# Kernel tuning notes

Hardware: AMD Instinct MI355X
Metric: run time of the kernel (lower is better)

Reference implementation:

```python
import jax, jax.numpy as jnp
import numpy as np

N, L, D = 4, 2048, 1024
H_DIM, OUT_DIM = 1024, 1024


def setup_inputs() -> dict:
    key = jax.random.key(0)
    ks = jax.random.split(key, 7)
    scale = 0.02
    return {
        "x": jax.random.normal(ks[0], (N, L, D), dtype=jnp.float32),
        "Wq": jax.random.normal(ks[1], (D, H_DIM), dtype=jnp.float32) * scale,
        "bq": jnp.zeros((H_DIM,), dtype=jnp.float32),
        "Wk": jax.random.normal(ks[2], (D, H_DIM), dtype=jnp.float32) * scale,
        "bk": jnp.zeros((H_DIM,), dtype=jnp.float32),
        "Wv": jax.random.normal(ks[3], (D, OUT_DIM), dtype=jnp.float32) * scale,
        "bv": jnp.zeros((OUT_DIM,), dtype=jnp.float32),
    }


def reference(x, Wq, bq, Wk, bk, Wv, bv):
    # q,k: [N,L,h_dim], v: [N,L,out_dim]
    q = jnp.einsum("nld,dh->nlh", x, Wq) + bq
    k = jnp.einsum("nld,dh->nlh", x, Wk) + bk
    v = jnp.einsum("nld,do->nlo", x, Wv) + bv
    # scores: [N,L,L]
    qk = jnp.einsum("nlh,nmh->nlm", q, k)
    # NOTE: original scales by sqrt(qk.shape[-1]) == sqrt(L) (seq len), not sqrt(h_dim)
    seq_len = qk.shape[-1]
    s = jax.nn.softmax(qk / jnp.sqrt(jnp.asarray(seq_len, dtype=qk.dtype)), axis=-1)
    return jnp.einsum("nlm,nmo->nlo", s, v)
```

## Files before the change

kernel.cpp:

```cpp
#include <hip/hip_runtime.h>
#include <hip/hip_bf16.h>


typedef __attribute__((ext_vector_type(8))) short bf16x8;
typedef __attribute__((ext_vector_type(4))) float f32x4;

#define AS_G(p) ((__attribute__((address_space(1))) void*)(p))
#define AS_L(p) ((__attribute__((address_space(3))) void*)(p))

__device__ __forceinline__ unsigned short f2bf(float f) {
  unsigned int u = __float_as_uint(f);
  unsigned int lsb = (u >> 16) & 1u;
  u += 0x7fffu + lsb;
  return (unsigned short)(u >> 16);
}

__device__ __forceinline__ float bf2f(unsigned short h) {
  return __uint_as_float(((unsigned int)h) << 16);
}


template <int EPI>
__global__ __launch_bounds__(256) void gemm64(
    const unsigned short* __restrict__ A, const unsigned short* __restrict__ B,
    float* __restrict__ Cf, long long sA, long long sB, long long sC,
    int K, int lda, int ldb, int ldc,
    unsigned short* __restrict__ u0, unsigned short* __restrict__ u1,
    unsigned short* __restrict__ u2,
    const float* __restrict__ f0, const float* __restrict__ f1,
    const float* __restrict__ f2,
    float* __restrict__ rsum, float scale)
{
  __shared__ unsigned short lA[128 * 64];
  __shared__ unsigned short lB[128 * 64];

  const int t = threadIdx.x;
  const int rowBase = blockIdx.y * 128;
  const int colBase = blockIdx.x * 128;
  A += (long long)blockIdx.z * sA;
  B += (long long)blockIdx.z * sB;

  const int l = t & 63;
  const int w = t >> 6;
  const int wrow = (w >> 1) * 64;
  const int wcol = (w & 1) * 64;
  const int q = l >> 4;
  const int r16 = l & 15;

  f32x4 acc[4][4] = {};

  const int r0 = t >> 3;
  const int goff = (((t & 7) ^ (r0 & 7)) << 3);

  for (int kt = 0; kt < K; kt += 64) {
    __syncthreads();
#pragma unroll
    for (int u = 0; u < 4; u++) {
      const int row = r0 + 32 * u;
      __builtin_amdgcn_global_load_lds(AS_G(A + (size_t)(rowBase + row) * lda + kt + goff),
                                       AS_L(lA + (t + 256 * u) * 8), 16, 0, 0);
      __builtin_amdgcn_global_load_lds(AS_G(B + (size_t)(colBase + row) * ldb + kt + goff),
                                       AS_L(lB + (t + 256 * u) * 8), 16, 0, 0);
    }
    __syncthreads();

#pragma unroll
    for (int ks = 0; ks < 2; ks++) {
      bf16x8 af[4], bfr[4];
#pragma unroll
      for (int i = 0; i < 4; i++) {
        const int s = ((ks * 4 + q) ^ (r16 & 7));
        af[i] = *(const bf16x8*)(lA + (wrow + i * 16 + r16) * 64 + s * 8);
      }
#pragma unroll
      for (int j = 0; j < 4; j++) {
        const int s = ((ks * 4 + q) ^ (r16 & 7));
        bfr[j] = *(const bf16x8*)(lB + (wcol + j * 16 + r16) * 64 + s * 8);
      }
#pragma unroll
      for (int i = 0; i < 4; i++)
#pragma unroll
        for (int j = 0; j < 4; j++)
          acc[i][j] = __builtin_amdgcn_mfma_f32_16x16x32_bf16(af[i], bfr[j], acc[i][j], 0, 0, 0);
    }
  }

  if (EPI == 1) {
    unsigned short* p16 = u0 + (long long)blockIdx.z * sC;
    float* rs = rsum + (long long)blockIdx.z * 2048;
#pragma unroll
    for (int i = 0; i < 4; i++) {
#pragma unroll
      for (int r = 0; r < 4; r++) {
        int row = rowBase + wrow + i * 16 + q * 4 + r;
        float rowpart = 0.f;
#pragma unroll
        for (int j = 0; j < 4; j++) {
          int col = colBase + wcol + j * 16 + r16;
          float e = __expf(acc[i][j][r] * scale);
          p16[(size_t)row * ldc + col] = f2bf(e);
          rowpart += e;
        }
#pragma unroll
        for (int m = 1; m < 16; m <<= 1) rowpart += __shfl_xor(rowpart, m);
        if (r16 == 0) atomicAdd(rs + row, rowpart);
      }
    }
  } else if (EPI == 2) {
    const int seg = colBase >> 10;
    if (seg < 2) {
      unsigned short* dst = seg ? u1 : u0;
      const float* bias = seg ? f1 : f0;
      const int cb = colBase & 1023;
#pragma unroll
      for (int i = 0; i < 4; i++) {
#pragma unroll
        for (int r = 0; r < 4; r++) {
          int row = rowBase + wrow + i * 16 + q * 4 + r;
#pragma unroll
          for (int j = 0; j < 4; j++) {
            int col = cb + wcol + j * 16 + r16;
            dst[(size_t)row * 1024 + col] = f2bf(acc[i][j][r] + bias[col]);
          }
        }
      }
    } else {
      const int ob = colBase - 2048;
#pragma unroll
      for (int i = 0; i < 4; i++) {
        int posBase = rowBase + wrow + i * 16 + q * 4;
        int b = posBase >> 11;
        int pos = posBase & 2047;
#pragma unroll
        for (int j = 0; j < 4; j++) {
          int o = ob + wcol + j * 16 + r16;
          float bias = f2[o];
          ushort4 pk;
          pk.x = f2bf(acc[i][j][0] + bias);
          pk.y = f2bf(acc[i][j][1] + bias);
          pk.z = f2bf(acc[i][j][2] + bias);
          pk.w = f2bf(acc[i][j][3] + bias);
          *(ushort4*)(u2 + ((size_t)((b << 10) + o) * 2048 + pos)) = pk;
        }
      }
    }
  } else {
    float* C = Cf + (long long)blockIdx.z * sC;
    const float* rs = rsum + (long long)blockIdx.z * 2048;
#pragma unroll
    for (int i = 0; i < 4; i++) {
#pragma unroll
      for (int r = 0; r < 4; r++) {
        int row = rowBase + wrow + i * 16 + q * 4 + r;
        float inv = 1.0f / rs[row];
#pragma unroll
        for (int j = 0; j < 4; j++) {
          int col = colBase + wcol + j * 16 + r16;
          C[(size_t)row * ldc + col] = acc[i][j][r] * inv;
        }
      }
    }
  }
}


__global__ __launch_bounds__(256) void cast_f32_to_bf16(
    const float* __restrict__ in, unsigned short* __restrict__ out, int n4,
    float* __restrict__ rzero, int nz4)
{
  int i = blockIdx.x * 256 + threadIdx.x;
  if (i < nz4) ((float4*)rzero)[i] = make_float4(0.f, 0.f, 0.f, 0.f);
  if (i >= n4) return;
  float4 v = ((const float4*)in)[i];
  ushort4 o;
  o.x = f2bf(v.x); o.y = f2bf(v.y); o.z = f2bf(v.z); o.w = f2bf(v.w);
  ((ushort4*)out)[i] = o;
}


__global__ __launch_bounds__(256) void wtrans(
    const float* __restrict__ Wq, const float* __restrict__ Wk,
    const float* __restrict__ Wv, unsigned short* __restrict__ WT)
{
  __shared__ float tile[32][33];
  const float* in = blockIdx.z == 0 ? Wq : (blockIdx.z == 1 ? Wk : Wv);
  unsigned short* out = WT + (size_t)blockIdx.z * 1024 * 1024;
  const int bc = blockIdx.x * 32;
  const int br = blockIdx.y * 32;
  const int tx = threadIdx.x;
  const int ty = threadIdx.y;
#pragma unroll
  for (int i = 0; i < 4; i++)
    tile[ty + i * 8][tx] = in[(size_t)(br + ty + i * 8) * 1024 + bc + tx];
  __syncthreads();
#pragma unroll
  for (int i = 0; i < 4; i++)
    out[(size_t)(bc + ty + i * 8) * 1024 + br + tx] = f2bf(tile[tx][ty + i * 8]);
}


extern "C" void kernel_launch(void* const* d_in, const int* in_sizes, int n_in,
                              void* d_out, int out_size, void* d_ws, size_t ws_size,
                              hipStream_t stream) {
  (void)in_sizes; (void)n_in; (void)out_size;

  const float* x  = (const float*)d_in[0];
  const float* Wq = (const float*)d_in[1];
  const float* bq = (const float*)d_in[2];
  const float* Wk = (const float*)d_in[3];
  const float* bk = (const float*)d_in[4];
  const float* Wv = (const float*)d_in[5];
  const float* bv = (const float*)d_in[6];
  float* out = (float*)d_out;

  const int Nb = 4, L = 2048, D = 1024, H = 1024, O = 1024;
  const int M = Nb * L;
  const int NQKV = 3 * H;

  char* ws = (char*)d_ws;
  size_t off = 0;
  unsigned short* xb = (unsigned short*)(ws + off); off += (size_t)M * D * 2;
  unsigned short* qb = (unsigned short*)(ws + off); off += (size_t)M * H * 2;
  unsigned short* kb = (unsigned short*)(ws + off); off += (size_t)M * H * 2;
  unsigned short* vt = (unsigned short*)(ws + off); off += (size_t)M * O * 2;
  unsigned short* WT = (unsigned short*)(ws + off); off += (size_t)NQKV * D * 2;
  unsigned short* P  = (unsigned short*)(ws + off); off += (size_t)Nb * L * L * 2;
  float* rsum = (float*)(ws + off); off += (size_t)Nb * L * 4;
  if (ws_size < off) return;

  dim3 blk256(256);

  cast_f32_to_bf16<<<(M * D / 4 + 255) / 256, blk256, 0, stream>>>(
      x, xb, M * D / 4, rsum, Nb * L / 4);

  wtrans<<<dim3(32, 32, 3), dim3(32, 8), 0, stream>>>(Wq, Wk, Wv, WT);

  gemm64<2><<<dim3(NQKV / 128, M / 128, 1), blk256, 0, stream>>>(
      xb, WT, nullptr, 0, 0, 0, D, D, D, 0,
      qb, kb, vt, bq, bk, bv, nullptr, 0.f);

  gemm64<1><<<dim3(L / 128, L / 128, Nb), blk256, 0, stream>>>(
      qb, kb, nullptr, (long long)L * H, (long long)L * H, (long long)L * L,
      H, H, H, L,
      P, nullptr, nullptr, nullptr, nullptr, nullptr,
      rsum, 0.022097086912079608f );

  gemm64<3><<<dim3(O / 128, L / 128, Nb), blk256, 0, stream>>>(
      P, vt, out, (long long)L * L, (long long)O * L, (long long)L * O,
      L, L, L, O,
      nullptr, nullptr, nullptr, nullptr, nullptr, nullptr,
      rsum, 0.f);
}
```

Baseline: 271.8 us.

## Fold Wq·Wkᵀ into a single matrix to drop the K projection

Rewrites the attention scores as x·(Wk^T Wq)·x^T, computing the 1024x1024 product matrix once and applying it to x instead of projecting both Q and K. Softmax-invariant row terms are discarded and the bias contribution is reduced to a per-key column term computed by two small matvec kernels. This removes one third of the projection GEMM work at the cost of an extra small GEMM, extra launches, and extra bf16 rounding of the fused weight matrix.

```diff
diff --git a/kernel.cpp b/kernel.cpp
--- a/kernel.cpp
+++ b/kernel.cpp
@@ -1,5 +1,6 @@
 #include <hip/hip_runtime.h>
 #include <hip/hip_bf16.h>
+
 
 
 typedef __attribute__((ext_vector_type(8))) short bf16x8;
@@ -26,9 +27,7 @@
     float* __restrict__ Cf, long long sA, long long sB, long long sC,
     int K, int lda, int ldb, int ldc,
     unsigned short* __restrict__ u0, unsigned short* __restrict__ u1,
-    unsigned short* __restrict__ u2,
     const float* __restrict__ f0, const float* __restrict__ f1,
-    const float* __restrict__ f2,
     float* __restrict__ rsum, float scale)
 {
   __shared__ unsigned short lA[128 * 64];
@@ -87,7 +86,8 @@
 
   if (EPI == 1) {
     unsigned short* p16 = u0 + (long long)blockIdx.z * sC;
-    float* rs = rsum + (long long)blockIdx.z * 2048;
+    float* rs = rsum + ((long long)blockIdx.z << 11);
+    const float* sb = f0 + ((long long)blockIdx.z << 11);
 #pragma unroll
     for (int i = 0; i < 4; i++) {
 #pragma unroll
@@ -97,7 +97,7 @@
 #pragma unroll
         for (int j = 0; j < 4; j++) {
           int col = colBase + wcol + j * 16 + r16;
-          float e = __expf(acc[i][j][r] * scale);
+          float e = __expf(acc[i][j][r] * scale + sb[col]);
           p16[(size_t)row * ldc + col] = f2bf(e);
           rowpart += e;
         }
@@ -106,12 +106,37 @@
         if (r16 == 0) atomicAdd(rs + row, rowpart);
       }
     }
-  } else if (EPI == 2) {
-    const int seg = colBase >> 10;
-    if (seg < 2) {
-      unsigned short* dst = seg ? u1 : u0;
-      const float* bias = seg ? f1 : f0;
-      const int cb = colBase & 1023;
+  } else if (EPI == 3) {
+    float* C = Cf + (long long)blockIdx.z * sC;
+    const float* rs = rsum + ((long long)blockIdx.z << 11);
+#pragma unroll
+    for (int i = 0; i < 4; i++) {
+#pragma unroll
+      for (int r = 0; r < 4; r++) {
+        int row = rowBase + wrow + i * 16 + q * 4 + r;
+        float inv = 1.0f / rs[row];
+#pragma unroll
+        for (int j = 0; j < 4; j++) {
+          int col = colBase + wcol + j * 16 + r16;
+          C[(size_t)row * ldc + col] = acc[i][j][r] * inv;
+        }
+      }
+    }
+  } else if (EPI == 4) {
+#pragma unroll
+    for (int i = 0; i < 4; i++) {
+#pragma unroll
+      for (int r = 0; r < 4; r++) {
+        int row = rowBase + wrow + i * 16 + q * 4 + r;
+#pragma unroll
+        for (int j = 0; j < 4; j++) {
+          int col = colBase + wcol + j * 16 + r16;
+          u0[(size_t)row * ldc + col] = f2bf(acc[i][j][r]);
+        }
+      }
+    }
+  } else {
+    if (colBase < 1024) {
 #pragma unroll
       for (int i = 0; i < 4; i++) {
 #pragma unroll
@@ -119,13 +144,13 @@
           int row = rowBase + wrow + i * 16 + q * 4 + r;
 #pragma unroll
           for (int j = 0; j < 4; j++) {
-            int col = cb + wcol + j * 16 + r16;
-            dst[(size_t)row * 1024 + col] = f2bf(acc[i][j][r] + bias[col]);
+            int col = colBase + wcol + j * 16 + r16;
+            u0[(size_t)row * 1024 + col] = f2bf(acc[i][j][r]);
           }
         }
       }
     } else {
-      const int ob = colBase - 2048;
+      const int ob = colBase - 1024;
 #pragma unroll
       for (int i = 0; i < 4; i++) {
         int posBase = rowBase + wrow + i * 16 + q * 4;
@@ -134,29 +159,13 @@
 #pragma unroll
         for (int j = 0; j < 4; j++) {
           int o = ob + wcol + j * 16 + r16;
-          float bias = f2[o];
+          float bias = f1[o];
           ushort4 pk;
           pk.x = f2bf(acc[i][j][0] + bias);
           pk.y = f2bf(acc[i][j][1] + bias);
           pk.z = f2bf(acc[i][j][2] + bias);
           pk.w = f2bf(acc[i][j][3] + bias);
-          *(ushort4*)(u2 + ((size_t)((b << 10) + o) * 2048 + pos)) = pk;
-        }
-      }
-    }
-  } else {
-    float* C = Cf + (long long)blockIdx.z * sC;
-    const float* rs = rsum + (long long)blockIdx.z * 2048;
-#pragma unroll
-    for (int i = 0; i < 4; i++) {
-#pragma unroll
-      for (int r = 0; r < 4; r++) {
-        int row = rowBase + wrow + i * 16 + q * 4 + r;
-        float inv = 1.0f / rs[row];
-#pragma unroll
-        for (int j = 0; j < 4; j++) {
-          int col = colBase + wcol + j * 16 + r16;
-          C[(size_t)row * ldc + col] = acc[i][j][r] * inv;
+          *(ushort4*)(u1 + ((size_t)((b << 10) + o) * 2048 + pos)) = pk;
         }
       }
     }
@@ -164,38 +173,77 @@
 }
 
 
-__global__ __launch_bounds__(256) void cast_f32_to_bf16(
-    const float* __restrict__ in, unsigned short* __restrict__ out, int n4,
-    float* __restrict__ rzero, int nz4)
+__global__ __launch_bounds__(256) void prep(
+    const float* __restrict__ x, unsigned short* __restrict__ xb,
+    const float* __restrict__ Wq, unsigned short* __restrict__ wqb,
+    const float* __restrict__ Wk, unsigned short* __restrict__ wkb,
+    float* __restrict__ rsum)
 {
   int i = blockIdx.x * 256 + threadIdx.x;
-  if (i < nz4) ((float4*)rzero)[i] = make_float4(0.f, 0.f, 0.f, 0.f);
-  if (i >= n4) return;
-  float4 v = ((const float4*)in)[i];
-  ushort4 o;
-  o.x = f2bf(v.x); o.y = f2bf(v.y); o.z = f2bf(v.z); o.w = f2bf(v.w);
-  ((ushort4*)out)[i] = o;
+  if (i < 2097152) {
+    float4 v = ((const float4*)x)[i];
+    ushort4 o;
+    o.x = f2bf(v.x); o.y = f2bf(v.y); o.z = f2bf(v.z); o.w = f2bf(v.w);
+    ((ushort4*)xb)[i] = o;
+  }
+  if (i < 262144) {
+    float4 v = ((const float4*)Wq)[i];
+    ushort4 o;
+    o.x = f2bf(v.x); o.y = f2bf(v.y); o.z = f2bf(v.z); o.w = f2bf(v.w);
+    ((ushort4*)wqb)[i] = o;
+    float4 u = ((const float4*)Wk)[i];
+    ushort4 p;
+    p.x = f2bf(u.x); p.y = f2bf(u.y); p.z = f2bf(u.z); p.w = f2bf(u.w);
+    ((ushort4*)wkb)[i] = p;
+  }
+  if (i < 2048) ((float4*)rsum)[i] = make_float4(0.f, 0.f, 0.f, 0.f);
 }
 
 
 __global__ __launch_bounds__(256) void wtrans(
-    const float* __restrict__ Wq, const float* __restrict__ Wk,
-    const float* __restrict__ Wv, unsigned short* __restrict__ WT)
+    const float* __restrict__ Wv, unsigned short* __restrict__ dst)
 {
   __shared__ float tile[32][33];
-  const float* in = blockIdx.z == 0 ? Wq : (blockIdx.z == 1 ? Wk : Wv);
-  unsigned short* out = WT + (size_t)blockIdx.z * 1024 * 1024;
   const int bc = blockIdx.x * 32;
   const int br = blockIdx.y * 32;
   const int tx = threadIdx.x;
   const int ty = threadIdx.y;
 #pragma unroll
   for (int i = 0; i < 4; i++)
-    tile[ty + i * 8][tx] = in[(size_t)(br + ty + i * 8) * 1024 + bc + tx];
+    tile[ty + i * 8][tx] = Wv[(size_t)(br + ty + i * 8) * 1024 + bc + tx];
   __syncthreads();
 #pragma unroll
   for (int i = 0; i < 4; i++)
-    out[(size_t)(bc + ty + i * 8) * 1024 + br + tx] = f2bf(tile[tx][ty + i * 8]);
+    dst[(size_t)(bc + ty + i * 8) * 1024 + br + tx] = f2bf(tile[tx][ty + i * 8]);
+}
+
+
+__global__ __launch_bounds__(256) void matvec_wb(
+    const float* __restrict__ Wk, const float* __restrict__ bq,
+    float* __restrict__ z)
+{
+  int w = threadIdx.x >> 6, l = threadIdx.x & 63;
+  int d = blockIdx.x * 4 + w;
+  const float* row = Wk + (size_t)d * 1024;
+  float s = 0.f;
+  for (int h = l; h < 1024; h += 64) s += row[h] * bq[h];
+#pragma unroll
+  for (int off = 32; off >= 1; off >>= 1) s += __shfl_xor(s, off);
+  if (l == 0) z[d] = s;
+}
+
+__global__ __launch_bounds__(256) void matvec_xz(
+    const unsigned short* __restrict__ xb, const float* __restrict__ z,
+    float* __restrict__ sbeta, float scale)
+{
+  int w = threadIdx.x >> 6, l = threadIdx.x & 63;
+  int m = blockIdx.x * 4 + w;
+  const unsigned short* row = xb + (size_t)m * 1024;
+  float s = 0.f;
+  for (int h = l; h < 1024; h += 64) s += bf2f(row[h]) * z[h];
+#pragma unroll
+  for (int off = 32; off >= 1; off >>= 1) s += __shfl_xor(s, off);
+  if (l == 0) sbeta[m] = s * scale;
 }
 
 
@@ -208,46 +256,53 @@
   const float* Wq = (const float*)d_in[1];
   const float* bq = (const float*)d_in[2];
   const float* Wk = (const float*)d_in[3];
-  const float* bk = (const float*)d_in[4];
   const float* Wv = (const float*)d_in[5];
   const float* bv = (const float*)d_in[6];
   float* out = (float*)d_out;
 
-  const int Nb = 4, L = 2048, D = 1024, H = 1024, O = 1024;
+  const int Nb = 4, L = 2048, D = 1024, O = 1024;
   const int M = Nb * L;
-  const int NQKV = 3 * H;
+  const float scale = 0.022097086912079608f;
 
   char* ws = (char*)d_ws;
   size_t off = 0;
-  unsigned short* xb = (unsigned short*)(ws + off); off += (size_t)M * D * 2;
-  unsigned short* qb = (unsigned short*)(ws + off); off += (size_t)M * H * 2;
-  unsigned short* kb = (unsigned short*)(ws + off); off += (size_t)M * H * 2;
-  unsigned short* vt = (unsigned short*)(ws + off); off += (size_t)M * O * 2;
-  unsigned short* WT = (unsigned short*)(ws + off); off += (size_t)NQKV * D * 2;
-  unsigned short* P  = (unsigned short*)(ws + off); off += (size_t)Nb * L * L * 2;
-  float* rsum = (float*)(ws + off); off += (size_t)Nb * L * 4;
+  unsigned short* xb  = (unsigned short*)(ws + off); off += (size_t)M * D * 2;
+  unsigned short* xg  = (unsigned short*)(ws + off); off += (size_t)M * D * 2;
+  unsigned short* vt  = (unsigned short*)(ws + off); off += (size_t)M * O * 2;
+  unsigned short* Bp  = (unsigned short*)(ws + off); off += (size_t)2048 * D * 2;
+  unsigned short* wqb = (unsigned short*)(ws + off); off += (size_t)D * D * 2;
+  unsigned short* wkb = (unsigned short*)(ws + off); off += (size_t)D * D * 2;
+  unsigned short* P   = (unsigned short*)(ws + off); off += (size_t)Nb * L * L * 2;
+  float* rsum  = (float*)(ws + off); off += (size_t)M * 4;
+  float* zvec  = (float*)(ws + off); off += (size_t)D * 4;
+  float* sbeta = (float*)(ws + off); off += (size_t)M * 4;
   if (ws_size < off) return;
 
   dim3 blk256(256);
 
-  cast_f32_to_bf16<<<(M * D / 4 + 255) / 256, blk256, 0, stream>>>(
-      x, xb, M * D / 4, rsum, Nb * L / 4);
-
-  wtrans<<<dim3(32, 32, 3), dim3(32, 8), 0, stream>>>(Wq, Wk, Wv, WT);
-
-  gemm64<2><<<dim3(NQKV / 128, M / 128, 1), blk256, 0, stream>>>(
-      xb, WT, nullptr, 0, 0, 0, D, D, D, 0,
-      qb, kb, vt, bq, bk, bv, nullptr, 0.f);
-
-  gemm64<1><<<dim3(L / 128, L / 128, Nb), blk256, 0, stream>>>(
-      qb, kb, nullptr, (long long)L * H, (long long)L * H, (long long)L * L,
-      H, H, H, L,
-      P, nullptr, nullptr, nullptr, nullptr, nullptr,
-      rsum, 0.022097086912079608f );
-
-  gemm64<3><<<dim3(O / 128, L / 128, Nb), blk256, 0, stream>>>(
+  prep<<<8192, blk256, 0, stream>>>(x, xb, Wq, wqb, Wk, wkb, rsum);
+
+  wtrans<<<dim3(32, 32, 1), dim3(32, 8), 0, stream>>>(Wv, Bp + (size_t)1024 * 1024);
+
+  matvec_wb<<<256, blk256, 0, stream>>>(Wk, bq, zvec);
+
+  gemm64<4><<<dim3(8, 8, 1), blk256, 0, stream>>>(
+      wkb, wqb, nullptr, 0, 0, 0, D, D, D, D,
+      Bp, nullptr, nullptr, nullptr, nullptr, 0.f);
+
+  matvec_xz<<<2048, blk256, 0, stream>>>(xb, zvec, sbeta, scale);
+
+  gemm64<5><<<dim3(16, 64, 1), blk256, 0, stream>>>(
+      xb, Bp, nullptr, 0, 0, 0, D, D, D, 0,
+      xg, vt, nullptr, bv, nullptr, 0.f);
+
+  gemm64<1><<<dim3(16, 16, 4), blk256, 0, stream>>>(
+      xg, xb, nullptr, (long long)L * D, (long long)L * D, (long long)L * L,
+      D, D, D, L,
+      P, nullptr, sbeta, nullptr, rsum, scale);
+
+  gemm64<3><<<dim3(8, 16, 4), blk256, 0, stream>>>(
       P, vt, out, (long long)L * L, (long long)O * L, (long long)L * O,
       L, L, L, O,
-      nullptr, nullptr, nullptr, nullptr, nullptr, nullptr,
-      rsum, 0.f);
-}
+      nullptr, nullptr, nullptr, nullptr, rsum, 0.f);
+}
```

Result: slower. 284.8 us (+4.8%).
